# Kernel tuning notes

Measured on AMD Instinct MI355X. Metric: run time of the kernel, lower is better.

The kernel has to match this reference:

```python
import jax, jax.numpy as jnp
import numpy as np

N_NODES = 50000
N_FEAT = 512
N_HID = 128
N_CLASS = 8
N_EDGES = 640000


def setup_inputs() -> dict:
    key = jax.random.key(0)
    k1, k2, k3, k4, k5 = jax.random.split(key, 5)
    x = jax.random.normal(k1, (N_NODES, N_FEAT), dtype=jnp.float32)
    edge_index = jax.random.randint(k2, (2, N_EDGES), 0, N_NODES, dtype=jnp.int64)
    # GCNConv linear weight (glorot), stored as [nfeat, nhid] for x @ W
    s_conv = jnp.sqrt(6.0 / (N_FEAT + N_HID)).astype(jnp.float32)
    W_conv = jax.random.uniform(k3, (N_FEAT, N_HID), jnp.float32, -s_conv, s_conv)
    b_conv = jnp.zeros((N_HID,), jnp.float32)
    # fc head, xavier_uniform per weights_init, bias zero
    s_fc = jnp.sqrt(6.0 / (N_HID + N_CLASS)).astype(jnp.float32)
    W_fc = jax.random.uniform(k4, (N_HID, N_CLASS), jnp.float32, -s_fc, s_fc)
    b_fc = jnp.zeros((N_CLASS,), jnp.float32)
    return {"x": x, "edge_index": edge_index, "W_conv": W_conv,
            "b_conv": b_conv, "W_fc": W_fc, "b_fc": b_fc}


def reference(x, edge_index, W_conv, b_conv, W_fc, b_fc):
    N = x.shape[0]
    # GCNConv: add self-loops, symmetric normalization deg^-1/2 A deg^-1/2
    loop = jnp.arange(N, dtype=edge_index.dtype)
    src = jnp.concatenate([edge_index[0], loop])  # [E+N]
    dst = jnp.concatenate([edge_index[1], loop])
    ones = jnp.ones(src.shape[0], dtype=x.dtype)
    deg = jax.ops.segment_sum(ones, dst, num_segments=N)  # in-degree incl. self loop
    dinv = jnp.where(deg > 0, jax.lax.rsqrt(deg), 0.0)
    norm = dinv[src] * dinv[dst]  # [E+N]
    h = x @ W_conv  # [N, nhid] dense transform before propagation
    msg = h[src] * norm[:, None]  # gather + scale, [E+N, nhid]
    out = jax.ops.segment_sum(msg, dst, num_segments=N) + b_conv  # scatter-add
    # linear classification head
    return out @ W_fc + b_fc  # [N, nclass]
```

## Files before the change

kernel.cpp:

```cpp
#include <hip/hip_runtime.h>
#include <hip/hip_bf16.h>

#define NFEAT 512
#define NCLS 8
#define NHID 128
#define NPB 16
#define NBIN 3125
#define NBIN16 3136
#define WINE 1024
#define NW 625
#define BINCAP 320
#define NODECAP 64
#define NHT 6250

typedef float4 f4;
typedef unsigned short u16;
typedef unsigned int u32;
typedef short bf16x8 __attribute__((ext_vector_type(8)));
typedef float f32x4 __attribute__((ext_vector_type(4)));

__device__ inline u16 f2bf(float f) {
    __hip_bfloat16 h = __float2bfloat16(f);
    u16 u; __builtin_memcpy(&u, &h, 2);
    return u;
}

__global__ __launch_bounds__(256) void histinit_kernel(
    const int* __restrict__ dst,
    const float* __restrict__ W1, const float* __restrict__ W2,
    const float* __restrict__ b1, const float* __restrict__ b2,
    u16* __restrict__ WbT, float* __restrict__ bias2,
    int* __restrict__ wincnt, int E)
{
    const int tid = threadIdx.x;
    const int bid = blockIdx.x;
    int t = bid * 256 + tid;
    if (t < NFEAT * NCLS) {
        int k = t >> 3, c = t & 7;
        const float* w1r = W1 + k * NHID;
        float acc = 0.f;
        #pragma unroll 8
        for (int j = 0; j < NHID; ++j) acc = fmaf(w1r[j], W2[j * NCLS + c], acc);
        WbT[c * NFEAT + k] = f2bf(acc);
        WbT[(c + 8) * NFEAT + k] = 0;
    }
    if (t < NCLS) {
        float acc = b2[t];
        for (int j = 0; j < NHID; ++j) acc = fmaf(b1[j], W2[j * NCLS + t], acc);
        bias2[t] = acc;
    }

    __shared__ int hist[NBIN16];
    for (int k = tid; k < NBIN16; k += 256) hist[k] = 0;
    __syncthreads();
    int e0 = bid * WINE;
    #pragma unroll
    for (int j = 0; j < 4; ++j) {
        int e = e0 + j * 256 + tid;
        if (e < E) atomicAdd(&hist[dst[e] >> 4], 1);
    }
    __syncthreads();
    int* row = wincnt + (size_t)bid * NBIN16;
    for (int k = tid; k < NBIN16; k += 256) row[k] = hist[k];
}

__global__ __launch_bounds__(256) void colprefix_kernel(
    int* __restrict__ wincnt, int* __restrict__ colsum)
{
    const int bg = blockIdx.x;
    const int t = threadIdx.x;
    const int bl = t & 15, chunk = t >> 4;
    const int CPW = (NW + 15) / 16;
    int vals[40];
    int s = 0;
    for (int k = 0; k < CPW; ++k) {
        int win = chunk * CPW + k;
        int v = (win < NW) ? wincnt[(size_t)win * NBIN16 + bg * 16 + bl] : 0;
        vals[k] = v; s += v;
    }
    __shared__ int part[256];
    part[bl * 16 + chunk] = s;
    __syncthreads();
    int base = 0;
    for (int c = 0; c < chunk; ++c) base += part[bl * 16 + c];
    int run = base;
    for (int k = 0; k < CPW; ++k) {
        int win = chunk * CPW + k;
        if (win < NW) {
            wincnt[(size_t)win * NBIN16 + bg * 16 + bl] = run;
            run += vals[k];
        }
    }
    if (chunk == 15) colsum[bg * 16 + bl] = run;
}

__global__ __launch_bounds__(256, 6) void mainfused_kernel(
    const int* __restrict__ src, const int* __restrict__ dst,
    const float* __restrict__ x, const u16* __restrict__ WbT,
    const int* __restrict__ wincnt, u32* __restrict__ ebuf,
    float* __restrict__ gp0, float* __restrict__ gp1, int N, int E)
{
    const int tid  = threadIdx.x;
    const int bid  = blockIdx.x;
    const int lane = tid & 63;
    const int r16  = lane & 15;
    const int g4   = lane >> 4;

    __shared__ int loff[NBIN16];
    __shared__ int rank[NBIN16];

    if (bid < NW) {
        const int* row = wincnt + (size_t)bid * NBIN16;
        for (int k = tid; k < NBIN16; k += 256) {
            loff[k] = row[k];
            rank[k] = 0;
        }
        __syncthreads();
        int e0 = bid * WINE;
        #pragma unroll
        for (int j = 0; j < 4; ++j) {
            int e = e0 + j * 256 + tid;
            if (e < E) {
                int d = dst[e];
                int b = d >> 4;
                int r = atomicAdd(&rank[b], 1);
                int pos = loff[b] + r;
                if (pos < BINCAP) {
                    u32 val = (u32)src[e] | ((u32)(d & 15) << 16);
                    __builtin_nontemporal_store(val, &ebuf[(size_t)b * BINCAP + pos]);
                }
            }
        }
    }

    const int ht = bid * 4 + (tid >> 6);
    if (ht >= NHT) return;
    const int tile = ht >> 1;
    const int half = ht & 1;
    const int row0 = tile * 16;
    const int k0   = half * 256;

    const float* xr = x + (size_t)(row0 + r16) * NFEAT + k0 + g4 * 8;
    const u16*   wp = WbT + r16 * NFEAT + k0 + g4 * 8;

    f32x4 acc = {0.f, 0.f, 0.f, 0.f};
    f4 p = *(const f4*)(xr);
    f4 q = *(const f4*)(xr + 4);
    #pragma unroll
    for (int ks = 0; ks < 8; ++ks) {
        f4 pn, qn;
        if (ks < 7) {
            pn = *(const f4*)(xr + (ks + 1) * 32);
            qn = *(const f4*)(xr + (ks + 1) * 32 + 4);
        }
        union { bf16x8 v; u16 u[8]; } af;
        af.u[0] = f2bf(p.x); af.u[1] = f2bf(p.y);
        af.u[2] = f2bf(p.z); af.u[3] = f2bf(p.w);
        af.u[4] = f2bf(q.x); af.u[5] = f2bf(q.y);
        af.u[6] = f2bf(q.z); af.u[7] = f2bf(q.w);
        bf16x8 bv = *(const bf16x8*)(wp + ks * 32);
        acc = __builtin_amdgcn_mfma_f32_16x16x32_bf16(af.v, bv, acc, 0, 0, 0);
        if (ks < 7) { p = pn; q = qn; }
    }
    float* gp = half ? gp1 : gp0;
    if (r16 < NCLS) {
        #pragma unroll
        for (int r = 0; r < 4; ++r)
            gp[(size_t)(row0 + g4 * 4 + r) * 8 + r16] = acc[r];
    }
}

__global__ __launch_bounds__(256) void degscale_kernel(
    const u32* __restrict__ ebuf, const int* __restrict__ colsum,
    const float* __restrict__ gp0, const float* __restrict__ gp1,
    float* __restrict__ g)
{
    const int tid = threadIdx.x;
    const int wv = tid >> 6, lane = tid & 63;
    const int bin = blockIdx.x * 4 + wv;
    if (bin >= NBIN) return;
    __shared__ int cnt_s[4][NPB];
    if (lane < NPB) cnt_s[wv][lane] = 0;
    __syncthreads();
    int cnt = min(colsum[bin], BINCAP);
    const u32* eb = ebuf + (size_t)bin * BINCAP;
    for (int k = lane; k < cnt; k += 64)
        atomicAdd(&cnt_s[wv][eb[k] >> 16], 1);
    __syncthreads();
    #pragma unroll
    for (int half = 0; half < 2; ++half) {
        int k2 = lane + half * 64;
        int node = k2 >> 3, c = k2 & 7;
        size_t i = (size_t)(bin * NPB + node) * 8 + c;
        float di = rsqrtf((float)cnt_s[wv][node] + 1.0f);
        g[i] = (gp0[i] + gp1[i]) * di;
    }
}

__global__ __launch_bounds__(256) void gather_kernel(
    const u32* __restrict__ ebuf, const int* __restrict__ colsum,
    const float* __restrict__ g, const float* __restrict__ bias2,
    float* __restrict__ out)
{
    const int tid = threadIdx.x;
    const int wv = tid >> 6, lane = tid & 63;
    const int bin = blockIdx.x * 4 + wv;
    if (bin >= NBIN) return;
    __shared__ u16 list[4][NPB][NODECAP];
    __shared__ int cnt_s[4][NPB];
    if (lane < NPB) cnt_s[wv][lane] = 0;
    __syncthreads();
    int cnt = min(colsum[bin], BINCAP);
    const u32* eb = ebuf + (size_t)bin * BINCAP;
    for (int k = lane; k < cnt; k += 64) {
        u32 u = eb[k];
        int node = u >> 16;
        int r = atomicAdd(&cnt_s[wv][node], 1);
        if (r < NODECAP) list[wv][node][r] = (u16)(u & 0xFFFF);
    }
    __syncthreads();
    #pragma unroll
    for (int half = 0; half < 2; ++half) {
        int k2 = lane + half * 64;
        int node = k2 >> 3, c = k2 & 7;
        int i = bin * NPB + node;
        int n = min(cnt_s[wv][node], NODECAP);
        float acc = 0.f;
        for (int k = 0; k < n; ++k) {
            int s = list[wv][node][k];
            acc += g[(size_t)s * 8 + c];
        }
        float di = rsqrtf((float)cnt_s[wv][node] + 1.0f);
        out[(size_t)i * 8 + c] = fmaf(di, acc + g[(size_t)i * 8 + c], bias2[c]);
    }
}

extern "C" void kernel_launch(void* const* d_in, const int* in_sizes, int n_in,
                              void* d_out, int out_size, void* d_ws, size_t ws_size,
                              hipStream_t stream)
{
    const float* x  = (const float*)d_in[0];
    const int*   ei = (const int*)d_in[1];
    const float* W1 = (const float*)d_in[2];
    const float* b1 = (const float*)d_in[3];
    const float* W2 = (const float*)d_in[4];
    const float* b2 = (const float*)d_in[5];
    float* out = (float*)d_out;

    const int N = in_sizes[0] / NFEAT;
    const int E = in_sizes[1] / 2;
    const int* src = ei;
    const int* dst = ei + E;

    char* ws = (char*)d_ws;
    size_t off = 0;
    auto alloc = [&](size_t bytes) {
        char* p = ws + off;
        off += (bytes + 255) & ~(size_t)255;
        return p;
    };
    int*   wincnt = (int*)alloc((size_t)NW * NBIN16 * 4);
    int*   colsum = (int*)alloc((size_t)NBIN16 * 4);
    u32*   ebuf   = (u32*)alloc((size_t)NBIN * BINCAP * 4);
    float* gp0    = (float*)alloc((size_t)N * 8 * 4);
    float* gp1    = (float*)alloc((size_t)N * 8 * 4);
    float* g      = (float*)alloc((size_t)N * 8 * 4);
    u16*   WbT    = (u16*)alloc((size_t)16 * NFEAT * 2);
    float* bias2  = (float*)alloc(NCLS * 4);

    const int MB = (NHT + 3) / 4;
    const int BB = (NBIN + 3) / 4;

    histinit_kernel<<<NW, 256, 0, stream>>>(dst, W1, W2, b1, b2, WbT, bias2, wincnt, E);

    colprefix_kernel<<<196, 256, 0, stream>>>(wincnt, colsum);

    mainfused_kernel<<<MB, 256, 0, stream>>>(src, dst, x, WbT, wincnt, ebuf, gp0, gp1, N, E);

    degscale_kernel<<<BB, 256, 0, stream>>>(ebuf, colsum, gp0, gp1, g);

    gather_kernel<<<BB, 256, 0, stream>>>(ebuf, colsum, g, bias2, out);
}
```

Baseline: 79.05 us.

## Split fused scatter+GEMM into separate kernels with hybrid MFMA/FP32 GEMM row split

```diff
diff --git a/kernel.cpp b/kernel.cpp
--- a/kernel.cpp
+++ b/kernel.cpp
@@ -11,7 +11,9 @@
 #define NW 625
 #define BINCAP 320
 #define NODECAP 64
-#define NHT 6250
+#define TILEA 1562
+#define ROWSPLIT (TILEA * 16)
+#define NQT (TILEA * 4)
 
 typedef float4 f4;
 typedef unsigned short u16;
@@ -29,7 +31,7 @@
     const int* __restrict__ dst,
     const float* __restrict__ W1, const float* __restrict__ W2,
     const float* __restrict__ b1, const float* __restrict__ b2,
-    u16* __restrict__ WbT, float* __restrict__ bias2,
+    float* __restrict__ W12, u16* __restrict__ WbT, float* __restrict__ bias2,
     int* __restrict__ wincnt, int E)
 {
     const int tid = threadIdx.x;
@@ -41,6 +43,7 @@
         float acc = 0.f;
         #pragma unroll 8
         for (int j = 0; j < NHID; ++j) acc = fmaf(w1r[j], W2[j * NCLS + c], acc);
+        W12[t] = acc;
         WbT[c * NFEAT + k] = f2bf(acc);
         WbT[(c + 8) * NFEAT + k] = 0;
     }
@@ -94,75 +97,69 @@
     if (chunk == 15) colsum[bg * 16 + bl] = run;
 }
 
-__global__ __launch_bounds__(256, 6) void mainfused_kernel(
+__global__ __launch_bounds__(256) void pass_kernel(
     const int* __restrict__ src, const int* __restrict__ dst,
-    const float* __restrict__ x, const u16* __restrict__ WbT,
-    const int* __restrict__ wincnt, u32* __restrict__ ebuf,
-    float* __restrict__ gp0, float* __restrict__ gp1, int N, int E)
-{
-    const int tid  = threadIdx.x;
-    const int bid  = blockIdx.x;
-    const int lane = tid & 63;
-    const int r16  = lane & 15;
-    const int g4   = lane >> 4;
-
+    const int* __restrict__ wincnt, u32* __restrict__ ebuf, int E)
+{
+    const int tid = threadIdx.x;
+    const int bid = blockIdx.x;
     __shared__ int loff[NBIN16];
     __shared__ int rank[NBIN16];
-
-    if (bid < NW) {
-        const int* row = wincnt + (size_t)bid * NBIN16;
-        for (int k = tid; k < NBIN16; k += 256) {
-            loff[k] = row[k];
-            rank[k] = 0;
-        }
-        __syncthreads();
-        int e0 = bid * WINE;
-        #pragma unroll
-        for (int j = 0; j < 4; ++j) {
-            int e = e0 + j * 256 + tid;
-            if (e < E) {
-                int d = dst[e];
-                int b = d >> 4;
-                int r = atomicAdd(&rank[b], 1);
-                int pos = loff[b] + r;
-                if (pos < BINCAP) {
-                    u32 val = (u32)src[e] | ((u32)(d & 15) << 16);
-                    __builtin_nontemporal_store(val, &ebuf[(size_t)b * BINCAP + pos]);
-                }
+    const int* row = wincnt + (size_t)bid * NBIN16;
+    for (int k = tid; k < NBIN16; k += 256) {
+        loff[k] = row[k];
+        rank[k] = 0;
+    }
+    __syncthreads();
+    int e0 = bid * WINE;
+    #pragma unroll
+    for (int j = 0; j < 4; ++j) {
+        int e = e0 + j * 256 + tid;
+        if (e < E) {
+            int d = dst[e];
+            int b = d >> 4;
+            int r = atomicAdd(&rank[b], 1);
+            int pos = loff[b] + r;
+            if (pos < BINCAP) {
+                u32 val = (u32)src[e] | ((u32)(d & 15) << 16);
+                __builtin_nontemporal_store(val, &ebuf[(size_t)b * BINCAP + pos]);
             }
         }
     }
-
-    const int ht = bid * 4 + (tid >> 6);
-    if (ht >= NHT) return;
-    const int tile = ht >> 1;
-    const int half = ht & 1;
-    const int row0 = tile * 16;
-    const int k0   = half * 256;
-
+}
+
+__global__ __launch_bounds__(256) void gemmA_kernel(
+    const float* __restrict__ x, const u16* __restrict__ WbT,
+    float* __restrict__ gp0, float* __restrict__ gp1,
+    float* __restrict__ gp2, float* __restrict__ gp3)
+{
+    const int lane = threadIdx.x & 63;
+    const int ht = blockIdx.x * 4 + (threadIdx.x >> 6);
+    if (ht >= NQT) return;
+    const int tile = ht >> 2, q = ht & 3;
+    const int row0 = tile * 16, k0 = q * 128;
+    const int r16 = lane & 15, g4 = lane >> 4;
     const float* xr = x + (size_t)(row0 + r16) * NFEAT + k0 + g4 * 8;
     const u16*   wp = WbT + r16 * NFEAT + k0 + g4 * 8;
 
+    f4 pb[4], qb[4];
+    #pragma unroll
+    for (int i = 0; i < 4; ++i) {
+        pb[i] = *(const f4*)(xr + i * 32);
+        qb[i] = *(const f4*)(xr + i * 32 + 4);
+    }
     f32x4 acc = {0.f, 0.f, 0.f, 0.f};
-    f4 p = *(const f4*)(xr);
-    f4 q = *(const f4*)(xr + 4);
-    #pragma unroll
-    for (int ks = 0; ks < 8; ++ks) {
-        f4 pn, qn;
-        if (ks < 7) {
-            pn = *(const f4*)(xr + (ks + 1) * 32);
-            qn = *(const f4*)(xr + (ks + 1) * 32 + 4);
-        }
+    #pragma unroll
+    for (int ks = 0; ks < 4; ++ks) {
         union { bf16x8 v; u16 u[8]; } af;
-        af.u[0] = f2bf(p.x); af.u[1] = f2bf(p.y);
-        af.u[2] = f2bf(p.z); af.u[3] = f2bf(p.w);
-        af.u[4] = f2bf(q.x); af.u[5] = f2bf(q.y);
-        af.u[6] = f2bf(q.z); af.u[7] = f2bf(q.w);
+        af.u[0] = f2bf(pb[ks].x); af.u[1] = f2bf(pb[ks].y);
+        af.u[2] = f2bf(pb[ks].z); af.u[3] = f2bf(pb[ks].w);
+        af.u[4] = f2bf(qb[ks].x); af.u[5] = f2bf(qb[ks].y);
+        af.u[6] = f2bf(qb[ks].z); af.u[7] = f2bf(qb[ks].w);
         bf16x8 bv = *(const bf16x8*)(wp + ks * 32);
         acc = __builtin_amdgcn_mfma_f32_16x16x32_bf16(af.v, bv, acc, 0, 0, 0);
-        if (ks < 7) { p = pn; q = qn; }
-    }
-    float* gp = half ? gp1 : gp0;
+    }
+    float* gp = (q == 0) ? gp0 : (q == 1) ? gp1 : (q == 2) ? gp2 : gp3;
     if (r16 < NCLS) {
         #pragma unroll
         for (int r = 0; r < 4; ++r)
@@ -170,9 +167,54 @@
     }
 }
 
+__global__ __launch_bounds__(256) void gemmB_kernel(
+    const float* __restrict__ x, const float* __restrict__ W12,
+    float* __restrict__ gp0, int N)
+{
+    int lane = threadIdx.x & 63;
+    int wave = (blockIdx.x * 256 + threadIdx.x) >> 6;
+    int nwaves = gridDim.x * 4;
+
+    float w[2][4][8];
+    #pragma unroll
+    for (int j = 0; j < 2; ++j)
+        #pragma unroll
+        for (int m = 0; m < 4; ++m) {
+            const f4* wp = (const f4*)(W12 + (j * 256 + lane * 4 + m) * 8);
+            f4 lo = wp[0], hi = wp[1];
+            w[j][m][0] = lo.x; w[j][m][1] = lo.y; w[j][m][2] = lo.z; w[j][m][3] = lo.w;
+            w[j][m][4] = hi.x; w[j][m][5] = hi.y; w[j][m][6] = hi.z; w[j][m][7] = hi.w;
+        }
+
+    for (int row = ROWSPLIT + wave; row < N; row += nwaves) {
+        const f4* xr = (const f4*)(x + (size_t)row * NFEAT);
+        f4 a0 = xr[lane];
+        f4 a1 = xr[lane + 64];
+        float acc[8];
+        #pragma unroll
+        for (int c = 0; c < 8; ++c) {
+            acc[c] = a0.x * w[0][0][c] + a0.y * w[0][1][c]
+                   + a0.z * w[0][2][c] + a0.w * w[0][3][c]
+                   + a1.x * w[1][0][c] + a1.y * w[1][1][c]
+                   + a1.z * w[1][2][c] + a1.w * w[1][3][c];
+        }
+        #pragma unroll
+        for (int d = 32; d >= 1; d >>= 1)
+            #pragma unroll
+            for (int c = 0; c < 8; ++c)
+                acc[c] += __shfl_xor(acc[c], d);
+        if (lane == 0) {
+            f4* go = (f4*)(gp0 + (size_t)row * 8);
+            go[0] = make_float4(acc[0], acc[1], acc[2], acc[3]);
+            go[1] = make_float4(acc[4], acc[5], acc[6], acc[7]);
+        }
+    }
+}
+
 __global__ __launch_bounds__(256) void degscale_kernel(
     const u32* __restrict__ ebuf, const int* __restrict__ colsum,
     const float* __restrict__ gp0, const float* __restrict__ gp1,
+    const float* __restrict__ gp2, const float* __restrict__ gp3,
     float* __restrict__ g)
 {
     const int tid = threadIdx.x;
@@ -192,8 +234,10 @@
         int k2 = lane + half * 64;
         int node = k2 >> 3, c = k2 & 7;
         size_t i = (size_t)(bin * NPB + node) * 8 + c;
+        float sum = gp0[i];
+        if (bin < TILEA) sum += gp1[i] + gp2[i] + gp3[i];
         float di = rsqrtf((float)cnt_s[wv][node] + 1.0f);
-        g[i] = (gp0[i] + gp1[i]) * di;
+        g[i] = sum * di;
     }
 }
 
@@ -264,20 +308,26 @@
     u32*   ebuf   = (u32*)alloc((size_t)NBIN * BINCAP * 4);
     float* gp0    = (float*)alloc((size_t)N * 8 * 4);
     float* gp1    = (float*)alloc((size_t)N * 8 * 4);
+    float* gp2    = (float*)alloc((size_t)N * 8 * 4);
+    float* gp3    = (float*)alloc((size_t)N * 8 * 4);
     float* g      = (float*)alloc((size_t)N * 8 * 4);
+    float* W12    = (float*)alloc(NFEAT * NCLS * 4);
     u16*   WbT    = (u16*)alloc((size_t)16 * NFEAT * 2);
     float* bias2  = (float*)alloc(NCLS * 4);
 
-    const int MB = (NHT + 3) / 4;
     const int BB = (NBIN + 3) / 4;
 
-    histinit_kernel<<<NW, 256, 0, stream>>>(dst, W1, W2, b1, b2, WbT, bias2, wincnt, E);
+    histinit_kernel<<<NW, 256, 0, stream>>>(dst, W1, W2, b1, b2, W12, WbT, bias2, wincnt, E);
 
     colprefix_kernel<<<196, 256, 0, stream>>>(wincnt, colsum);
 
-    mainfused_kernel<<<MB, 256, 0, stream>>>(src, dst, x, WbT, wincnt, ebuf, gp0, gp1, N, E);
-
-    degscale_kernel<<<BB, 256, 0, stream>>>(ebuf, colsum, gp0, gp1, g);
+    pass_kernel<<<NW, 256, 0, stream>>>(src, dst, wincnt, ebuf, E);
+
+    gemmA_kernel<<<(NQT + 3) / 4, 256, 0, stream>>>(x, WbT, gp0, gp1, gp2, gp3);
+
+    gemmB_kernel<<<2048, 256, 0, stream>>>(x, W12, gp0, N);
+
+    degscale_kernel<<<BB, 256, 0, stream>>>(ebuf, colsum, gp0, gp1, gp2, gp3, g);
 
     gather_kernel<<<BB, 256, 0, stream>>>(ebuf, colsum, g, bias2, out);
 }
```

Result: slower. 98.07 us (+24.1%).
